# Kernel tuning notes

Hardware: AMD Instinct MI355X
Metric: run time of the kernel (lower is better)

## Reference

```python
import jax, jax.numpy as jnp
import numpy as np

OUT_FEATURES = 4096
IN_FEATURES = 4096
GROUP_SIZE = 16


def setup_inputs() -> dict:
    key = jax.random.key(0)
    k1, k2, k3, k4 = jax.random.split(key, 4)
    n_groups = OUT_FEATURES * IN_FEATURES // GROUP_SIZE
    x = jax.random.normal(k1, (8, 2048, IN_FEATURES), dtype=jnp.float32)
    weight_q = jax.random.randint(k2, (n_groups, GROUP_SIZE), 0, 16, dtype=jnp.int32).astype(jnp.int8)
    weight_norm = jax.random.uniform(k3, (n_groups, 1), dtype=jnp.float32).astype(jnp.float16)
    bias = jax.random.normal(k4, (OUT_FEATURES,), dtype=jnp.float32)
    return {"x": x, "weight_q": weight_q, "weight_norm": weight_norm, "bias": bias}


def reference(x, weight_q, weight_norm, bias):
    # block dequant: (q/15) * per-group scale, then reshape to [out, in]
    w = (weight_q.astype(jnp.float32) / 15.0) * weight_norm.astype(jnp.float32)
    w = w.reshape(OUT_FEATURES, IN_FEATURES)
    # F.linear: x @ w^T + bias
    return jnp.einsum('bsi,oi->bso', x, w) + bias
```

## Files before the change

### kernel.cpp

```cpp
#include <hip/hip_runtime.h>

#define MDIM 16384
#define NDIM 4096
#define KDIM 4096
#define NT   64

typedef unsigned short u16;
typedef unsigned int   u32;
typedef __attribute__((ext_vector_type(8))) short bh8;
typedef __attribute__((ext_vector_type(4))) float f32x4;
typedef __attribute__((ext_vector_type(4))) int   i32x4;

__device__ __forceinline__ u16 f2bf(float f) {
  u32 u = __builtin_bit_cast(u32, f);
  u = (u + 0x7fffu + ((u >> 16) & 1u)) >> 16;
  return (u16)u;
}

__device__ __forceinline__ void gld16(const void* g, const void* lds) {
  __builtin_amdgcn_global_load_lds((const __attribute__((address_space(1))) u32*)g,
                                   (__attribute__((address_space(3))) u32*)lds, 16, 0, 0);
}

__global__ void cvt_x(const float* __restrict__ x, u16* __restrict__ xb) {
  size_t i = ((size_t)blockIdx.x * 256 + threadIdx.x) * 8;
  f32x4 a = *(const f32x4*)(x + i);
  f32x4 b = *(const f32x4*)(x + i + 4);
  bh8 o;
  o[0] = (short)f2bf(a[0]); o[1] = (short)f2bf(a[1]);
  o[2] = (short)f2bf(a[2]); o[3] = (short)f2bf(a[3]);
  o[4] = (short)f2bf(b[0]); o[5] = (short)f2bf(b[1]);
  o[6] = (short)f2bf(b[2]); o[7] = (short)f2bf(b[3]);
  *(bh8*)(xb + i) = o;
}

__global__ void deq_w(const int* __restrict__ qi, const void* __restrict__ nrm,
                      u16* __restrict__ wb) {
  __shared__ int s_q8, s_n32;
  if (threadIdx.x == 0) {
    int packed = 0;
    for (int t = 0; t < 64; ++t) { unsigned v = (unsigned)qi[t]; if (v > 15u) packed = 1; }
    int n32 = 0;
    const u16* h = (const u16*)nrm;
    for (int t = 0; t < 64; ++t) { u16 b = h[t]; if (b < 0x8000u && b > 0x3C00u) n32 = 1; }
    s_q8 = packed; s_n32 = n32;
  }
  __syncthreads();
  const bool q8 = (s_q8 != 0), n32 = (s_n32 != 0);

  int g = blockIdx.x * 256 + threadIdx.x;
  float s;
  if (n32) s = ((const float*)nrm)[g] * (1.0f / 15.0f);
  else {
    u16 hb = ((const u16*)nrm)[g];
    s = (float)__builtin_bit_cast(_Float16, hb) * (1.0f / 15.0f);
  }
  float q[16];
  if (q8) {
    i32x4 v = *(const i32x4*)((const unsigned char*)qi + (size_t)g * 16);
#pragma unroll
    for (int k = 0; k < 4; ++k) {
      int word = v[k];
      q[k*4+0] = (float)(word & 255);        q[k*4+1] = (float)((word >> 8) & 255);
      q[k*4+2] = (float)((word >> 16) & 255); q[k*4+3] = (float)((word >> 24) & 255);
    }
  } else {
    const i32x4* p = (const i32x4*)(qi + (size_t)g * 16);
#pragma unroll
    for (int k = 0; k < 4; ++k) {
      i32x4 v = p[k];
      q[k*4+0] = (float)v[0]; q[k*4+1] = (float)v[1];
      q[k*4+2] = (float)v[2]; q[k*4+3] = (float)v[3];
    }
  }
  bh8 o0, o1;
#pragma unroll
  for (int j = 0; j < 8; ++j) o0[j] = (short)f2bf(q[j] * s);
#pragma unroll
  for (int j = 0; j < 8; ++j) o1[j] = (short)f2bf(q[8 + j] * s);
  *(bh8*)(wb + (size_t)g * 16) = o0;
  *(bh8*)(wb + (size_t)g * 16 + 8) = o1;
}

__global__ __launch_bounds__(512, 2) void gemm8(const u16* __restrict__ A,
                                                const u16* __restrict__ B,
                                                const float* __restrict__ bias,
                                                float* __restrict__ out) {
  __shared__ u16 lds[65536];
  const int tid = threadIdx.x;
  const int w = tid >> 6, l = tid & 63;
  const int wm = w >> 2, wn = w & 3;

  int bid = blockIdx.x;
  int wg = (bid & 7) * 128 + (bid >> 3);
  const int bm = wg >> 4;
  const int bn = wg & 15;

  const int cs8  = ((l & 7) ^ (l >> 3)) * 8;
  const u16* aSrc = A + (size_t)(bm * 256 + w * 32 + (l >> 3)) * 4096 + cs8;
  const u16* bSrc = B + (size_t)(bn * 256 + w * 32 + (l >> 3)) * 4096 + cs8;

  const int fr  = (l & 15) * 64;
  const int sz0 = (((l >> 4)) ^ (l & 7)) * 8;
  const int sz1 = ((4 + (l >> 4)) ^ (l & 7)) * 8;

  f32x4 acc[8][4];
#pragma unroll
  for (int mi = 0; mi < 8; ++mi)
#pragma unroll
    for (int ni = 0; ni < 4; ++ni) acc[mi][ni] = (f32x4){0.f, 0.f, 0.f, 0.f};

  bh8 af[4][2], b0f[2][2], b1f[2][2];

  auto STG = [&](int op, int h, int kt) {
    const u16* s = (op ? bSrc : aSrc) + h * 65536 + kt * 64;
    int d = (op ? 32768 : 0) + ((kt & 1) * 2 + h) * 8192 + w * 1024;
    gld16(s,         &lds[d]);
    gld16(s + 32768, &lds[d + 512]);
  };
  auto RDA = [&](int buf, int mp) {
#pragma unroll
    for (int q = 0; q < 4; ++q) {
      int base = (buf * 2 + mp) * 8192 + (wm * 4 + q) * 1024 + fr;
      af[q][0] = *(const bh8*)&lds[base + sz0];
      af[q][1] = *(const bh8*)&lds[base + sz1];
    }
  };
  auto RDB = [&](int buf, int np, bh8 (&bb)[2][2]) {
#pragma unroll
    for (int q = 0; q < 2; ++q) {
      int base = 32768 + (buf * 2 + np) * 8192 + (wn * 2 + q) * 1024 + fr;
      bb[q][0] = *(const bh8*)&lds[base + sz0];
      bb[q][1] = *(const bh8*)&lds[base + sz1];
    }
  };
  auto MM = [&](int mp, int np, bh8 (&bb)[2][2]) {
    __builtin_amdgcn_s_setprio(1);
#pragma unroll
    for (int q = 0; q < 4; ++q)
#pragma unroll
      for (int r = 0; r < 2; ++r)
#pragma unroll
        for (int kk = 0; kk < 2; ++kk)
          acc[q*2+mp][r*2+np] = __builtin_amdgcn_mfma_f32_16x16x32_bf16(
              af[q][kk], bb[r][kk], acc[q*2+mp][r*2+np], 0, 0, 0);
    __builtin_amdgcn_s_setprio(0);
  };

#define PH(BUF, MP, NP, BB, RA, RB, PRE) \
  do { \
    if (RA) RDA(BUF, MP); \
    if (RB) RDB(BUF, NP, BB); \
    PRE \
    __builtin_amdgcn_s_barrier(); \
    asm volatile("s_waitcnt lgkmcnt(0)"); \
    __builtin_amdgcn_sched_barrier(0); \
    MM(MP, NP, BB); \
    __builtin_amdgcn_s_barrier(); \
  } while (0)

  STG(0, 0, 0); STG(1, 0, 0); STG(0, 1, 0); STG(1, 1, 0);
  STG(0, 0, 1); STG(1, 0, 1); STG(0, 1, 1); STG(1, 1, 1);
  asm volatile("s_waitcnt vmcnt(8)");
  __builtin_amdgcn_s_barrier();

#pragma unroll 1
  for (int i = 0; i < NT / 2 - 1; ++i) {
    const int c = 2 * i + 2, d = 2 * i + 3;
    PH(0, 0, 0, b0f, 1, 1, {});
    PH(0, 0, 1, b1f, 0, 1, { STG(0, 0, c); STG(1, 0, c); });
    PH(0, 1, 0, b0f, 1, 0, { STG(1, 1, c); });
    PH(0, 1, 1, b1f, 0, 0, { STG(0, 1, c); asm volatile("s_waitcnt vmcnt(8)"); });
    PH(1, 0, 0, b0f, 1, 1, {});
    PH(1, 0, 1, b1f, 0, 1, { STG(0, 0, d); STG(1, 0, d); });
    PH(1, 1, 0, b0f, 1, 0, { STG(1, 1, d); });
    PH(1, 1, 1, b1f, 0, 0, { STG(0, 1, d); asm volatile("s_waitcnt vmcnt(8)"); });
  }
  PH(0, 0, 0, b0f, 1, 1, {});
  PH(0, 0, 1, b1f, 0, 1, {});
  PH(0, 1, 0, b0f, 1, 0, {});
  PH(0, 1, 1, b1f, 0, 0, { asm volatile("s_waitcnt vmcnt(0)"); });
  PH(1, 0, 0, b0f, 1, 1, {});
  PH(1, 0, 1, b1f, 0, 1, {});
  PH(1, 1, 0, b0f, 1, 0, {});
  PH(1, 1, 1, b1f, 0, 0, {});
#undef PH

  const int col0 = bn * 256 + wn * 64 + (l & 15);
  const int row0 = bm * 256 + wm * 128 + (l >> 4) * 4;
#pragma unroll
  for (int ni = 0; ni < 4; ++ni) {
    float bv = bias[col0 + ni * 16];
#pragma unroll
    for (int mi = 0; mi < 8; ++mi) {
      size_t base = (size_t)(row0 + mi * 16) * 4096 + (size_t)(col0 + ni * 16);
#pragma unroll
      for (int rr = 0; rr < 4; ++rr)
        out[base + (size_t)rr * 4096] = acc[mi][ni][rr] + bv;
    }
  }
}

__global__ __launch_bounds__(512, 2) void gemm_fb(const float* __restrict__ Af32,
                                                  const u16* __restrict__ Wbf,
                                                  const float* __restrict__ bias,
                                                  float* __restrict__ out) {
  __shared__ u16 lds[65536];
  const int tid = threadIdx.x;
  const int w = tid >> 6, l = tid & 63;
  const int wm = w >> 2, wn = w & 3;
  int bid = blockIdx.x;
  int wg = (bid & 7) * 128 + (bid >> 3);
  const int bm = wg >> 4, bn = wg & 15;

  int srcOffB[4], srcOffA32[4], dstSwzA[4];
#pragma unroll
  for (int j = 0; j < 4; ++j) {
    int ci = (w * 4 + j) * 64 + l;
    int r = ci >> 3, c = ci & 7;
    int cs = c ^ (r & 7);
    srcOffB[j]   = (bn * 256 + r) * 4096 + cs * 8;
    srcOffA32[j] = (bm * 256 + r) * 4096 + c * 8;
    dstSwzA[j]   = r * 64 + cs * 8;
  }
  const int ar = wm * 128 + (l & 15);
  const int br = wn * 64 + (l & 15);
  const int swz0 = (((l >> 4) + 0) ^ (l & 7)) * 8;
  const int swz1 = (((l >> 4) + 4) ^ (l & 7)) * 8;
  const int aoff0 = ar * 64 + swz0, aoff1 = ar * 64 + swz1;
  const int boff0 = 32768 + br * 64 + swz0, boff1 = 32768 + br * 64 + swz1;

  f32x4 acc[8][4];
#pragma unroll
  for (int mi = 0; mi < 8; ++mi)
#pragma unroll
    for (int ni = 0; ni < 4; ++ni) acc[mi][ni] = (f32x4){0.f, 0.f, 0.f, 0.f};

  auto STAGE = [&](int bufb, int kt) {
    const int kof = kt * 64;
#pragma unroll
    for (int j = 0; j < 4; ++j) {
      gld16(Wbf + srcOffB[j] + kof, &lds[32768 + bufb * 16384 + (w * 4 + j) * 512]);
      const float* p = Af32 + srcOffA32[j] + kof;
      f32x4 v0 = *(const f32x4*)p;
      f32x4 v1 = *(const f32x4*)(p + 4);
      bh8 o;
      o[0] = (short)f2bf(v0[0]); o[1] = (short)f2bf(v0[1]);
      o[2] = (short)f2bf(v0[2]); o[3] = (short)f2bf(v0[3]);
      o[4] = (short)f2bf(v1[0]); o[5] = (short)f2bf(v1[1]);
      o[6] = (short)f2bf(v1[2]); o[7] = (short)f2bf(v1[3]);
      *(bh8*)&lds[bufb * 16384 + dstSwzA[j]] = o;
    }
  };
  auto COMPUTE = [&](int bufb) {
    const int ab = bufb * 16384;
#pragma unroll
    for (int kk = 0; kk < 2; ++kk) {
      const int ao = ab + (kk ? aoff1 : aoff0);
      const int bo = ab + (kk ? boff1 : boff0);
      bh8 afr[8], bfr[4];
#pragma unroll
      for (int mi = 0; mi < 8; ++mi) afr[mi] = *(const bh8*)&lds[ao + mi * 1024];
#pragma unroll
      for (int ni = 0; ni < 4; ++ni) bfr[ni] = *(const bh8*)&lds[bo + ni * 1024];
#pragma unroll
      for (int mi = 0; mi < 8; ++mi)
#pragma unroll
        for (int ni = 0; ni < 4; ++ni)
          acc[mi][ni] = __builtin_amdgcn_mfma_f32_16x16x32_bf16(afr[mi], bfr[ni],
                                                                acc[mi][ni], 0, 0, 0);
    }
  };

  int buf = 0;
  STAGE(0, 0);
  __syncthreads();
  for (int kt = 0; kt < NT - 1; ++kt) {
    STAGE(buf ^ 1, kt + 1);
    COMPUTE(buf);
    __syncthreads();
    buf ^= 1;
  }
  COMPUTE(buf);

  const int col0 = bn * 256 + wn * 64 + (l & 15);
  const int row0 = bm * 256 + wm * 128 + (l >> 4) * 4;
#pragma unroll
  for (int ni = 0; ni < 4; ++ni) {
    float bv = bias[col0 + ni * 16];
#pragma unroll
    for (int mi = 0; mi < 8; ++mi) {
      size_t base = (size_t)(row0 + mi * 16) * 4096 + (size_t)(col0 + ni * 16);
#pragma unroll
      for (int rr = 0; rr < 4; ++rr)
        out[base + (size_t)rr * 4096] = acc[mi][ni][rr] + bv;
    }
  }
}

extern "C" void kernel_launch(void* const* d_in, const int* in_sizes, int n_in,
                              void* d_out, int out_size, void* d_ws, size_t ws_size,
                              hipStream_t stream) {
  const float* x    = (const float*)d_in[0];
  const int*   wq   = (const int*)d_in[1];
  const void*  wn   = d_in[2];
  const float* bias = (const float*)d_in[3];
  float*       out  = (float*)d_out;

  const size_t needA = (size_t)MDIM * KDIM * 2;
  const size_t needW = (size_t)NDIM * KDIM * 2;

  if (ws_size >= needA + needW) {
    u16* xbf = (u16*)d_ws;
    u16* wbf = (u16*)((char*)d_ws + needA);
    cvt_x<<<dim3(32768), dim3(256), 0, stream>>>(x, xbf);
    deq_w<<<dim3(4096), dim3(256), 0, stream>>>(wq, wn, wbf);
    gemm8<<<dim3(1024), dim3(512), 0, stream>>>(xbf, wbf, bias, out);
  } else if (ws_size >= needW) {
    u16* wbf = (u16*)d_ws;
    deq_w<<<dim3(4096), dim3(256), 0, stream>>>(wq, wn, wbf);
    gemm_fb<<<dim3(1024), dim3(512), 0, stream>>>(x, wbf, bias, out);
  }
}
```

Before: 566.9 us.

## Restructure GEMM main loop to double-buffer A fragments and overlap LDS reads with MFMA

Rewrites the bf16 GEMM inner schedule. All B fragments for a k-tile are now read once, and A fragments are read in four 32-row chunks ping-ponged between two register sets, so the next chunk's LDS reads are issued before the current chunk's MFMAs. The explicit lgkmcnt waits and sched_barrier are removed, and global-to-LDS stages are reordered with adjusted vmcnt thresholds. This is meant to hide LDS latency behind matrix work and cut per-phase stalls. It relies on the compiler inserting correct waits and risks races from the changed barrier and vmcnt placement, plus higher register pressure.

```diff
diff --git a/kernel.cpp b/kernel.cpp
--- a/kernel.cpp
+++ b/kernel.cpp
@@ -101,7 +101,7 @@
   const u16* bSrc = B + (size_t)(bn * 256 + w * 32 + (l >> 3)) * 4096 + cs8;
 
   const int fr  = (l & 15) * 64;
-  const int sz0 = (((l >> 4)) ^ (l & 7)) * 8;
+  const int sz0 = ((l >> 4) ^ (l & 7)) * 8;
   const int sz1 = ((4 + (l >> 4)) ^ (l & 7)) * 8;
 
   f32x4 acc[8][4];
@@ -110,7 +110,8 @@
 #pragma unroll
     for (int ni = 0; ni < 4; ++ni) acc[mi][ni] = (f32x4){0.f, 0.f, 0.f, 0.f};
 
-  bh8 af[4][2], b0f[2][2], b1f[2][2];
+  bh8 aX[2][2], aY[2][2];
+  bh8 bf_[4][2];
 
   auto STG = [&](int op, int h, int kt) {
     const u16* s = (op ? bSrc : aSrc) + h * 65536 + kt * 64;
@@ -118,73 +119,81 @@
     gld16(s,         &lds[d]);
     gld16(s + 32768, &lds[d + 512]);
   };
-  auto RDA = [&](int buf, int mp) {
-#pragma unroll
-    for (int q = 0; q < 4; ++q) {
-      int base = (buf * 2 + mp) * 8192 + (wm * 4 + q) * 1024 + fr;
-      af[q][0] = *(const bh8*)&lds[base + sz0];
-      af[q][1] = *(const bh8*)&lds[base + sz1];
-    }
-  };
-  auto RDB = [&](int buf, int np, bh8 (&bb)[2][2]) {
+  auto RDA = [&](int buf, int mb, bh8 (&aa)[2][2]) {
 #pragma unroll
     for (int q = 0; q < 2; ++q) {
-      int base = 32768 + (buf * 2 + np) * 8192 + (wn * 2 + q) * 1024 + fr;
-      bb[q][0] = *(const bh8*)&lds[base + sz0];
-      bb[q][1] = *(const bh8*)&lds[base + sz1];
-    }
-  };
-  auto MM = [&](int mp, int np, bh8 (&bb)[2][2]) {
+      int base = (buf * 2 + q) * 8192 + (wm * 4 + mb) * 1024 + fr;
+      aa[q][0] = *(const bh8*)&lds[base + sz0];
+      aa[q][1] = *(const bh8*)&lds[base + sz1];
+    }
+  };
+  auto RDB = [&](int buf) {
+#pragma unroll
+    for (int r = 0; r < 4; ++r) {
+      int base = 32768 + (buf * 2 + (r & 1)) * 8192 + (wn * 2 + (r >> 1)) * 1024 + fr;
+      bf_[r][0] = *(const bh8*)&lds[base + sz0];
+      bf_[r][1] = *(const bh8*)&lds[base + sz1];
+    }
+  };
+  auto MMB = [&](int mb, bh8 (&aa)[2][2]) {
     __builtin_amdgcn_s_setprio(1);
 #pragma unroll
-    for (int q = 0; q < 4; ++q)
-#pragma unroll
-      for (int r = 0; r < 2; ++r)
-#pragma unroll
-        for (int kk = 0; kk < 2; ++kk)
-          acc[q*2+mp][r*2+np] = __builtin_amdgcn_mfma_f32_16x16x32_bf16(
-              af[q][kk], bb[r][kk], acc[q*2+mp][r*2+np], 0, 0, 0);
+    for (int kk = 0; kk < 2; ++kk)
+#pragma unroll
+      for (int q = 0; q < 2; ++q)
+#pragma unroll
+        for (int r = 0; r < 4; ++r)
+          acc[mb*2+q][r] = __builtin_amdgcn_mfma_f32_16x16x32_bf16(
+              aa[q][kk], bf_[r][kk], acc[mb*2+q][r], 0, 0, 0);
     __builtin_amdgcn_s_setprio(0);
   };
 
-#define PH(BUF, MP, NP, BB, RA, RB, PRE) \
-  do { \
-    if (RA) RDA(BUF, MP); \
-    if (RB) RDB(BUF, NP, BB); \
-    PRE \
-    __builtin_amdgcn_s_barrier(); \
-    asm volatile("s_waitcnt lgkmcnt(0)"); \
-    __builtin_amdgcn_sched_barrier(0); \
-    MM(MP, NP, BB); \
-    __builtin_amdgcn_s_barrier(); \
-  } while (0)
-
-  STG(0, 0, 0); STG(1, 0, 0); STG(0, 1, 0); STG(1, 1, 0);
-  STG(0, 0, 1); STG(1, 0, 1); STG(0, 1, 1); STG(1, 1, 1);
+#define BAR1 __builtin_amdgcn_s_barrier(); asm volatile("" ::: "memory");
+#define BAR2 __builtin_amdgcn_s_barrier();
+
+  STG(1, 0, 0); STG(1, 1, 0); STG(0, 0, 0); STG(0, 1, 0);
+  STG(1, 0, 1); STG(1, 1, 1); STG(0, 0, 1); STG(0, 1, 1);
   asm volatile("s_waitcnt vmcnt(8)");
-  __builtin_amdgcn_s_barrier();
+  BAR1;
+  RDA(0, 0, aX);
 
 #pragma unroll 1
   for (int i = 0; i < NT / 2 - 1; ++i) {
     const int c = 2 * i + 2, d = 2 * i + 3;
-    PH(0, 0, 0, b0f, 1, 1, {});
-    PH(0, 0, 1, b1f, 0, 1, { STG(0, 0, c); STG(1, 0, c); });
-    PH(0, 1, 0, b0f, 1, 0, { STG(1, 1, c); });
-    PH(0, 1, 1, b1f, 0, 0, { STG(0, 1, c); asm volatile("s_waitcnt vmcnt(8)"); });
-    PH(1, 0, 0, b0f, 1, 1, {});
-    PH(1, 0, 1, b1f, 0, 1, { STG(0, 0, d); STG(1, 0, d); });
-    PH(1, 1, 0, b0f, 1, 0, { STG(1, 1, d); });
-    PH(1, 1, 1, b1f, 0, 0, { STG(0, 1, d); asm volatile("s_waitcnt vmcnt(8)"); });
-  }
-  PH(0, 0, 0, b0f, 1, 1, {});
-  PH(0, 0, 1, b1f, 0, 1, {});
-  PH(0, 1, 0, b0f, 1, 0, {});
-  PH(0, 1, 1, b1f, 0, 0, { asm volatile("s_waitcnt vmcnt(0)"); });
-  PH(1, 0, 0, b0f, 1, 1, {});
-  PH(1, 0, 1, b1f, 0, 1, {});
-  PH(1, 1, 0, b0f, 1, 0, {});
-  PH(1, 1, 1, b1f, 0, 0, {});
-#undef PH
+    RDB(0); RDA(0, 1, aY);
+    BAR1; MMB(0, aX); BAR2;
+    RDA(0, 2, aX); STG(1, 0, c);
+    BAR1; MMB(1, aY); BAR2;
+    RDA(0, 3, aY); STG(1, 1, c);
+    BAR1; MMB(2, aX); BAR2;
+    STG(0, 0, c); asm volatile("s_waitcnt vmcnt(6)");
+    BAR1; RDA(1, 0, aX); MMB(3, aY); BAR2;
+    RDB(1); RDA(1, 1, aY); STG(0, 1, c);
+    BAR1; MMB(0, aX); BAR2;
+    RDA(1, 2, aX); STG(1, 0, d);
+    BAR1; MMB(1, aY); BAR2;
+    RDA(1, 3, aY); STG(1, 1, d);
+    BAR1; MMB(2, aX); BAR2;
+    STG(0, 0, d); STG(0, 1, d); asm volatile("s_waitcnt vmcnt(8)");
+    BAR1; RDA(0, 0, aX); MMB(3, aY); BAR2;
+  }
+  RDB(0); RDA(0, 1, aY);
+  BAR1; MMB(0, aX); BAR2;
+  RDA(0, 2, aX);
+  BAR1; MMB(1, aY); BAR2;
+  RDA(0, 3, aY);
+  BAR1; MMB(2, aX); BAR2;
+  asm volatile("s_waitcnt vmcnt(0)");
+  BAR1; RDA(1, 0, aX); MMB(3, aY); BAR2;
+  RDB(1); RDA(1, 1, aY);
+  BAR1; MMB(0, aX); BAR2;
+  RDA(1, 2, aX);
+  BAR1; MMB(1, aY); BAR2;
+  RDA(1, 3, aY);
+  BAR1; MMB(2, aX); BAR2;
+  BAR1; MMB(3, aY);
+#undef BAR1
+#undef BAR2
 
   const int col0 = bn * 256 + wn * 64 + (l & 15);
   const int row0 = bm * 256 + wm * 128 + (l >> 4) * 4;
```

Measured after the change: 544.7 us. -3.9%, faster.
